# Performance work log

Hardware: AMD Instinct MI355X
Metric: run time of the kernel (lower is better)

The kernel has to match this reference:

```python
import jax, jax.numpy as jnp
import numpy as np

# Dims (match init_kwargs / input_specs)
B, N, DIM, HEADS, DHEAD, CHUNK = 1, 2048, 1024, 8, 128, 64
HID = 4 * DHEAD            # MemoryMLP expansion_factor=4.0
DI = HEADS * DHEAD         # dim_inner
EPS = 1e-6
MAX_LR = 1.0               # default_step_transform_max_lr


def rmsnorm(x, w):
    return x * jax.lax.rsqrt(jnp.mean(jnp.square(x), -1, keepdims=True) + EPS) * w


def mem_forward(w0, w1, g, x):
    # ResidualNorm(MemoryMLP): y = RMSNorm(gelu(x@w0)@w1)*g + x
    h = jax.nn.gelu(x @ w0, approximate=False) @ w1
    return rmsnorm(h, g) + x


def setup_inputs() -> dict:
    key = jax.random.key(0)
    ks = jax.random.split(key, 12)
    s = lambda i, shape, sc: jax.random.normal(ks[i], shape, jnp.float32) * sc
    return dict(
        x=s(0, (B, N, DIM), 1.0),
        store_norm_w=jnp.ones((DIM,), jnp.float32),
        ret_norm_w=jnp.ones((DIM,), jnp.float32),
        Wq=s(1, (DIM, DI), DIM ** -0.5),
        Wk=s(2, (DIM, DI), DIM ** -0.5),
        Wv=s(3, (DIM, DI), DIM ** -0.5),
        W_step=s(4, (DIM, HEADS), DIM ** -0.5), b_step=jnp.zeros((HEADS,), jnp.float32),
        W_mom=s(5, (DIM, HEADS), DIM ** -0.5), b_mom=jnp.zeros((HEADS,), jnp.float32),
        W_decay=s(6, (DIM, HEADS), DIM ** -0.5), b_decay=jnp.zeros((HEADS,), jnp.float32),
        gate_W=s(7, (DIM, HEADS), DIM ** -0.5),
        combine_W=s(8, (DI, DIM), DI ** -0.5),
        mem_w0=s(9, (HEADS, DHEAD, HID), DHEAD ** -0.5),
        mem_w1=s(10, (HEADS, HID, DHEAD), HID ** -0.5),
        mem_g=jnp.ones((HEADS, DHEAD), jnp.float32),
    )


def reference(x, store_norm_w, ret_norm_w, Wq, Wk, Wv, W_step, b_step,
              W_mom, b_mom, W_decay, b_decay, gate_W, combine_W,
              mem_w0, mem_w1, mem_g):
    b, n, _ = x.shape
    nc = n // CHUNK
    BH = b * HEADS

    # ---- store path ----
    s = rmsnorm(x, store_norm_w)                                 # b n dim
    lr = jax.nn.sigmoid(s @ W_step + b_step) * MAX_LR            # b n h (per-token adaptive step)
    pooled = s.reshape(b, nc, CHUNK, DIM).mean(2)                # b nc dim (AveragePool chunk rep)
    mom = jax.nn.sigmoid(pooled @ W_mom + b_mom)                 # b nc h
    dec = jax.nn.sigmoid(pooled @ W_decay + b_decay)             # b nc h

    def to_chunks(t):  # b n (h d) -> (b h) nc c d
        return t.reshape(b, nc, CHUNK, HEADS, DHEAD).transpose(0, 3, 1, 2, 4).reshape(BH, nc, CHUNK, DHEAD)

    k = to_chunks(s @ Wk)
    v = to_chunks(s @ Wv)
    lr_c = lr.reshape(b, nc, CHUNK, HEADS).transpose(0, 3, 1, 2).reshape(BH, nc, CHUNK)
    mom_bh = mom.transpose(0, 2, 1).reshape(BH, nc)
    dec_bh = dec.transpose(0, 2, 1).reshape(BH, nc)

    # init fast weights per (b h)  (per_head_learned_parameters=True)
    w0 = jnp.broadcast_to(mem_w0[None], (b, HEADS, DHEAD, HID)).reshape(BH, DHEAD, HID)
    w1 = jnp.broadcast_to(mem_w1[None], (b, HEADS, HID, DHEAD)).reshape(BH, HID, DHEAD)
    g = jnp.broadcast_to(mem_g[None], (b, HEADS, DHEAD)).reshape(BH, DHEAD)

    def chunk_loss(w0_, w1_, g_, kc, vc, lrc):
        pred = mem_forward(w0_, w1_, g_, kc)                     # c d
        return jnp.sum(jnp.mean(jnp.square(pred - vc), -1) * lrc)

    grad_chunk = jax.grad(chunk_loss, argnums=(0, 1, 2))
    # vmap over chunks (same weights per chunk, per-sample grads), then over (b h)
    grads = jax.vmap(jax.vmap(grad_chunk, in_axes=(None, None, None, 0, 0, 0)))(w0, w1, g, k, v, lr_c)
    surprises = tuple(-gr for gr in grads)                       # each (BH, nc, ...)

    def combine(a, c):
        ga, xa = a
        gb, xb = c
        return (ga * gb, gb * xa + xb)

    def lin_scan(gates, xs):
        # y_i = gates_i * y_{i-1} + xs_i over chunk axis (axis=1)
        return jax.lax.associative_scan(combine, (gates, xs), axis=1)

    def expand(gates, ref):
        return gates.reshape(gates.shape + (1,) * (ref.ndim - 2))

    # momentum scan per parameter tensor
    updates = tuple(lin_scan(expand(mom_bh, su), su)[1] for su in surprises)

    # weight update scan: W_i = (1 - decay_i) * W_{i-1} + momentum_i, W_{-1} = init
    per_chunk_weights = []
    for upd, w_init in zip(updates, (w0, w1, g)):
        gates = expand(1.0 - dec_bh, upd)
        cumg, y = lin_scan(gates, upd)
        w_seq = y + cumg * w_init[:, None]                       # (BH, nc, ...)
        # retrieval at chunk i uses weights updated through chunk i-1
        per_chunk_weights.append(jnp.concatenate([w_init[:, None], w_seq[:, :-1]], axis=1))
    w0_c, w1_c, g_c = per_chunk_weights

    # ---- retrieve path ----
    r = rmsnorm(x, ret_norm_w)
    q = to_chunks(r @ Wq)                                        # (BH, nc, c, d)
    pred = jax.vmap(jax.vmap(mem_forward))(w0_c, w1_c, g_c, q)   # (BH, nc, c, d)
    out = pred.reshape(b, HEADS, n, DHEAD)                       # b h n d
    gate = jax.nn.sigmoid(r @ gate_W)                            # b n h (retrieve_gate, heads>1)
    out = out * gate.transpose(0, 2, 1)[..., None]
    out = out.transpose(0, 2, 1, 3).reshape(b, n, DI) @ combine_W
    return out
```

## Files before the change

### kernel.cpp

```cpp
#include <hip/hip_runtime.h>
#include <hip/hip_bf16.h>
#include <math.h>

#define NH   8
#define DHD  128
#define HIDN 512
#define CHK  64
#define NCH  32
#define MB   1048576ull

typedef unsigned short u16;
typedef unsigned int   u32;
typedef short s16x8 __attribute__((ext_vector_type(8)));
typedef float f32x4 __attribute__((ext_vector_type(4)));

#define MFMA(a,b,c) __builtin_amdgcn_mfma_f32_16x16x32_bf16((a),(b),(c),0,0,0)

__device__ __forceinline__ float bf2f(u16 v){ return __uint_as_float(((u32)v) << 16); }
__device__ __forceinline__ u16 f2bf(float f){
  u32 u = __float_as_uint(f);
  u += 0x7fffu + ((u >> 16) & 1u);
  return (u16)(u >> 16);
}
__device__ __forceinline__ u32 pack2(float a, float b){
  return (u32)f2bf(a) | ((u32)f2bf(b) << 16);
}
__device__ __forceinline__ float waveRedSum(float v){
  #pragma unroll
  for (int off = 32; off; off >>= 1) v += __shfl_xor(v, off);
  return v;
}
__device__ __forceinline__ int swzb(int row, int colb){ return colb ^ ((row & 7) << 4); }
__device__ __forceinline__ int swza(int row, int colb){
  return colb ^ ((row & 7) << 4) ^ (((row >> 3) & 3) << 5);
}



__global__ __launch_bounds__(256) void k_rmsnorm(const float* __restrict__ x,
    const float* __restrict__ wst, const float* __restrict__ wrt,
    u16* __restrict__ s_bf, u16* __restrict__ r_bf){
  int row = blockIdx.x, t = threadIdx.x;
  float4 v = ((const float4*)(x + (size_t)row*1024))[t];
  float ss = v.x*v.x + v.y*v.y + v.z*v.z + v.w*v.w;
  ss = waveRedSum(ss);
  __shared__ float red[4];
  int wv = t >> 6, ln = t & 63;
  if (ln == 0) red[wv] = ss;
  __syncthreads();
  float rr = rsqrtf((red[0]+red[1]+red[2]+red[3])*(1.f/1024.f) + 1e-6f);
  float4 a = ((const float4*)wst)[t];
  float4 b = ((const float4*)wrt)[t];
  uint2 so = make_uint2(pack2(v.x*rr*a.x, v.y*rr*a.y), pack2(v.z*rr*a.z, v.w*rr*a.w));
  uint2 ro = make_uint2(pack2(v.x*rr*b.x, v.y*rr*b.y), pack2(v.z*rr*b.z, v.w*rr*b.w));
  *(uint2*)(s_bf + (size_t)row*1024 + t*4) = so;
  *(uint2*)(r_bf + (size_t)row*1024 + t*4) = ro;
}

__global__ __launch_bounds__(256) void k_pool(const u16* __restrict__ s_bf, float* __restrict__ pooled){
  int c = blockIdx.x; int d = blockIdx.y*256 + threadIdx.x;
  float acc = 0.f;
  for (int tt = 0; tt < 64; ++tt) acc += bf2f(s_bf[((size_t)c*64+tt)*1024 + d]);
  pooled[(size_t)c*1024 + d] = acc * (1.f/64.f);
}

__global__ __launch_bounds__(256) void k_lrgate(const u16* __restrict__ s_bf, const u16* __restrict__ r_bf,
    const float* __restrict__ Wstep, const float* __restrict__ bstep,
    const float* __restrict__ gateW,
    float* __restrict__ lrc, float* __restrict__ gate){
  int wv = threadIdx.x >> 6, ln = threadIdx.x & 63;
  int tok = blockIdx.x*4 + wv;
  const u16* srow = s_bf + (size_t)tok*1024;
  const u16* rrow = r_bf + (size_t)tok*1024;
  for (int o = 0; o < 16; ++o){
    int h = o & 7;
    const u16* src = (o < 8) ? srow : rrow;
    const float* W = (o < 8) ? Wstep : gateW;
    float acc = 0.f;
    for (int k = ln; k < 1024; k += 64) acc += bf2f(src[k])*W[(size_t)k*8+h];
    acc = waveRedSum(acc);
    if (ln == 0){
      if (o < 8){
        float v = 1.f/(1.f+expf(-(acc + bstep[h])));
        lrc[((size_t)h*NCH + (tok>>6))*CHK + (tok&63)] = v;
      } else {
        gate[(size_t)tok*8 + h] = 1.f/(1.f+expf(-acc));
      }
    }
  }
}

__global__ __launch_bounds__(64) void k_momdec(const float* __restrict__ pooled,
    const float* __restrict__ Wmom, const float* __restrict__ bmom,
    const float* __restrict__ Wdec, const float* __restrict__ bdec,
    float* __restrict__ momb, float* __restrict__ decb){
  int c = blockIdx.x, ln = threadIdx.x;
  const float* prow = pooled + (size_t)c*1024;
  for (int o = 0; o < 16; ++o){
    int h = o & 7;
    const float* W = (o < 8) ? Wmom : Wdec;
    float acc = 0.f;
    for (int k = ln; k < 1024; k += 64) acc += prow[k]*W[(size_t)k*8+h];
    acc = waveRedSum(acc);
    if (ln == 0){
      float bb = (o < 8) ? bmom[h] : bdec[h];
      float v = 1.f/(1.f+expf(-(acc+bb)));
      if (o < 8) momb[h*NCH + c] = v; else decb[h*NCH + c] = v;
    }
  }
}

__global__ __launch_bounds__(256) void k_trf4(
    const float* __restrict__ A0, const float* __restrict__ A1,
    const float* __restrict__ A2, const float* __restrict__ A3,
    u16* __restrict__ O0, u16* __restrict__ O1, u16* __restrict__ O2, u16* __restrict__ O3){
  __shared__ u16 tile[32][34];
  int z = blockIdx.z;
  const float* in = (z==0)?A0:(z==1)?A1:(z==2)?A2:A3;
  u16* out = (z==0)?O0:(z==1)?O1:(z==2)?O2:O3;
  int c0 = blockIdx.x*32, r0 = blockIdx.y*32;
  int tx = threadIdx.x & 31, ty = threadIdx.x >> 5;
  #pragma unroll
  for (int k = 0; k < 4; ++k) tile[ty+k*8][tx] = f2bf(in[(size_t)(r0+ty+k*8)*1024 + c0+tx]);
  __syncthreads();
  #pragma unroll
  for (int k = 0; k < 4; ++k) out[(size_t)(c0+ty+k*8)*1024 + r0+tx] = tile[tx][ty+k*8];
}

__global__ __launch_bounds__(256) void k_packw(const float* __restrict__ mw0, const float* __restrict__ mw1,
    u16* __restrict__ w0L, u16* __restrict__ w1L, u16* __restrict__ w1bL){
  int h = blockIdx.z, which = blockIdx.y;
  int i = blockIdx.x*256 + threadIdx.x;
  int r = i & 511, blk = i >> 9;
  int lg = r >> 7, lr = (r >> 3) & 15, e = r & 7;
  float v; u16* dst;
  if (which == 0){ int n0 = blk >> 2, ks = blk & 3; int hid = n0*16+lr, d = ks*32+lg*8+e;
    v = mw0[(size_t)h*65536 + (size_t)d*512 + hid]; dst = w0L; }
  else if (which == 1){ int n0 = blk >> 4, ks = blk & 15; int d = n0*16+lr, hid = ks*32+lg*8+e;
    v = mw1[(size_t)h*65536 + (size_t)hid*128 + d]; dst = w1L; }
  else { int n0 = blk >> 2, ks = blk & 3; int hid = n0*16+lr, d = ks*32+lg*8+e;
    v = mw1[(size_t)h*65536 + (size_t)hid*128 + d]; dst = w1bL; }
  dst[(size_t)h*65536 + i] = f2bf(v);
}

__device__ __forceinline__ void gemm_body(const u16* __restrict__ A, const u16* __restrict__ BT,
    void* __restrict__ Cp, int mode){
  __shared__ char As[8192];
  __shared__ char Bs[8192];
  int t = threadIdx.x; int l = t & 63, w = t >> 6, lr16 = l & 15, lg = l >> 4;
  int bm = blockIdx.x*64, bn = blockIdx.y*64;
  f32x4 acc[4];
  #pragma unroll
  for (int mt = 0; mt < 4; ++mt) acc[mt] = (f32x4){0.f,0.f,0.f,0.f};
  for (int k0 = 0; k0 < 1024; k0 += 64){
    #pragma unroll
    for (int i = 0; i < 2; ++i){ int e = (i*256+t)*8; int row = e>>6, col = e&63;
      *(s16x8*)(As + row*128 + swzb(row, col*2)) = *(const s16x8*)(A + (size_t)(bm+row)*1024 + k0 + col);
      *(s16x8*)(Bs + row*128 + swzb(row, col*2)) = *(const s16x8*)(BT + (size_t)(bn+row)*1024 + k0 + col); }
    __syncthreads();
    #pragma unroll
    for (int ks = 0; ks < 2; ++ks){
      int rowb = w*16 + lr16;
      s16x8 y = *(const s16x8*)(Bs + rowb*128 + swzb(rowb, (ks*32+lg*8)*2));
      #pragma unroll
      for (int mt = 0; mt < 4; ++mt){ int row = mt*16 + lr16;
        s16x8 xa = *(const s16x8*)(As + row*128 + swzb(row, (ks*32+lg*8)*2));
        acc[mt] = MFMA(xa, y, acc[mt]); }
    }
    __syncthreads();
  }
  #pragma unroll
  for (int mt = 0; mt < 4; ++mt)
    #pragma unroll
    for (int j = 0; j < 4; ++j){
      int row = bm + mt*16 + lg*4 + j;
      int coln = bn + w*16 + lr16;
      if (mode == 0) ((float*)Cp)[(size_t)row*1024 + coln] = acc[mt][j];
      else { int cI = row>>6, tok = row&63, h = coln>>7, d = coln&127;
        ((u16*)Cp)[((size_t)(h*32+cI)*64 + tok)*128 + d] = f2bf(acc[mt][j]); }
    }
}

__global__ __launch_bounds__(256) void k_gemm_bf(const u16* __restrict__ A, const u16* __restrict__ BT,
    void* __restrict__ Cp, int mode){ gemm_body(A, BT, Cp, mode); }

__global__ __launch_bounds__(256) void k_gemm3(
    const u16* __restrict__ s_bf, const u16* __restrict__ r_bf,
    const u16* __restrict__ WkT, const u16* __restrict__ WvT, const u16* __restrict__ WqT,
    u16* __restrict__ Kc, u16* __restrict__ Vc, u16* __restrict__ Qc){
  int z = blockIdx.z;
  const u16* A = (z==2) ? r_bf : s_bf;
  const u16* BT = (z==0) ? WkT : (z==1) ? WvT : WqT;
  u16* C = (z==0) ? Kc : (z==1) ? Vc : Qc;
  gemm_body(A, BT, (void*)C, 1);
}

__global__ __launch_bounds__(512) void k_grad(
    const u16* __restrict__ Kc, const u16* __restrict__ Vc, const float* __restrict__ lrc,
    const u16* __restrict__ w0L, const u16* __restrict__ w1L, const u16* __restrict__ w1bL,
    const float* __restrict__ mg,
    u16* __restrict__ SW0, u16* __restrict__ SW1, float* __restrict__ SG){
  extern __shared__ char sm[];
  char* a_s   = sm;
  char* upT_s = sm + 65536;
  char* dh_s  = sm + 131072;
  char* dhT_s = sm + 147456;
  char* duT_s = a_s;
  char* kcT_s = upT_s;
  char* stg3  = dh_s;
  float* scr  = (float*)dh_s;

  int c = blockIdx.x, bh = blockIdx.y, t = threadIdx.x;
  size_t bc = (size_t)bh*NCH + c;
  int l = t & 63, w = t >> 6, lr16 = l & 15, lg = l >> 4;
  int tg = w & 3, dhf = w >> 2;
  int tokb = tg*16, tok0 = tokb + lg*4;

  const u16* kc_g = Kc + bc*8192;
  const u16* vc_g = Vc + bc*8192;

  s16x8 xk[4];
  #pragma unroll
  for (int k = 0; k < 4; ++k)
    xk[k] = *(const s16x8*)(kc_g + (size_t)(tokb+lr16)*128 + k*32 + lg*8);
  const u16* w0Lh = w0L + (size_t)bh*65536;
  for (int n0h = 0; n0h < 16; ++n0h){
    int n0 = dhf*16 + n0h;
    f32x4 acc = {0.f,0.f,0.f,0.f};
    const u16* yb = w0Lh + (size_t)n0*2048 + l*8;
    #pragma unroll
    for (int k = 0; k < 4; ++k) acc = MFMA(xk[k], *(const s16x8*)(yb + k*512), acc);
    int hid = n0*16 + lr16;
    float upv[4];
    #pragma unroll
    for (int j = 0; j < 4; ++j){
      int tok = tok0 + j;
      float u = acc[j];
      float cdf = 0.5f*(1.f + erff(u*0.70710678118654752f));
      upv[j] = cdf + u*0.3989422804014327f*expf(-0.5f*u*u);
      *(u16*)(a_s + tok*1024 + swza(tok, hid*2)) = f2bf(u*cdf);
    }
    *(uint2*)(upT_s + hid*128 + swzb(hid, tok0*2)) =
        make_uint2(pack2(upv[0], upv[1]), pack2(upv[2], upv[3]));
  }
  __syncthreads();

  s16x8 xa[16];
  #pragma unroll
  for (int k = 0; k < 16; ++k){ int row = tokb + lr16;
    xa[k] = *(const s16x8*)(a_s + row*1024 + swza(row, (k*32+lg*8)*2)); }
  const u16* w1Lh = w1L + (size_t)bh*65536;
  f32x4 hD[4];
  #pragma unroll
  for (int n0l = 0; n0l < 4; ++n0l){
    f32x4 acc = {0.f,0.f,0.f,0.f};
    const u16* yb = w1Lh + (size_t)(dhf*4 + n0l)*8192 + l*8;
    #pragma unroll
    for (int k = 0; k < 16; ++k) acc = MFMA(xa[k], *(const s16x8*)(yb + k*512), acc);
    hD[n0l] = acc;
  }
  #pragma unroll
  for (int j = 0; j < 4; ++j){
    float s = 0.f;
    #pragma unroll
    for (int n0l = 0; n0l < 4; ++n0l) s += hD[n0l][j]*hD[n0l][j];
    s += __shfl_xor(s,1); s += __shfl_xor(s,2); s += __shfl_xor(s,4); s += __shfl_xor(s,8);
    if (lr16 == 0) scr[dhf*64 + tok0 + j] = s;
  }
  __syncthreads();
  float rv[4], lrv[4], dotp[4];
  #pragma unroll
  for (int j = 0; j < 4; ++j){
    int tok = tok0 + j;
    float tot = scr[tok] + scr[64 + tok];
    rv[j] = rsqrtf(tot*(1.f/128.f) + 1e-6f);
    lrv[j] = lrc[bc*64 + tok];
    dotp[j] = 0.f;
  }
  float dn[4][4];
  #pragma unroll
  for (int n0l = 0; n0l < 4; ++n0l){
    int d = dhf*64 + n0l*16 + lr16;
    float g0 = mg[(size_t)bh*128 + d];
    float dgav = 0.f;
    #pragma unroll
    for (int j = 0; j < 4; ++j){
      int tok = tok0 + j;
      float h = hD[n0l][j];
      float nrm = h*rv[j];
      float kcv = bf2f(kc_g[(size_t)tok*128 + d]);
      float vcv = bf2f(vc_g[(size_t)tok*128 + d]);
      float p = nrm*g0 + kcv;
      float dp = (2.f/128.f)*lrv[j]*(p - vcv);
      dgav += dp*nrm;
      float dnv = dp*g0;
      dn[n0l][j] = dnv;
      dotp[j] += dnv*h;
    }
    dgav += __shfl_xor(dgav,16); dgav += __shfl_xor(dgav,32);
    if (lg == 0) scr[256 + w*64 + n0l*16 + lr16] = dgav;
  }
  #pragma unroll
  for (int j = 0; j < 4; ++j){
    float dd = dotp[j];
    dd += __shfl_xor(dd,1); dd += __shfl_xor(dd,2); dd += __shfl_xor(dd,4); dd += __shfl_xor(dd,8);
    if (lr16 == 0) scr[128 + dhf*64 + tok0 + j] = dd;
  }
  __syncthreads();
  float dotv[4];
  #pragma unroll
  for (int j = 0; j < 4; ++j){
    int tok = tok0 + j;
    dotv[j] = scr[128 + tok] + scr[128 + 64 + tok];
  }
  if (t < 128){
    int dh2 = t >> 6, dl = t & 63;
    float s = scr[256 + (dh2*4+0)*64 + dl] + scr[256 + (dh2*4+1)*64 + dl]
            + scr[256 + (dh2*4+2)*64 + dl] + scr[256 + (dh2*4+3)*64 + dl];
    SG[bc*128 + t] = -s;
  }
  __syncthreads();
  #pragma unroll
  for (int n0l = 0; n0l < 4; ++n0l){
    int d = dhf*64 + n0l*16 + lr16;
    float dhv[4];
    #pragma unroll
    for (int j = 0; j < 4; ++j){
      int tok = tok0 + j;
      float c3 = rv[j]*rv[j]*rv[j]*(1.f/128.f);
      dhv[j] = rv[j]*dn[n0l][j] - c3*dotv[j]*hD[n0l][j];
      *(u16*)(dh_s + tok*256 + swzb(tok, d*2)) = f2bf(dhv[j]);
    }
    *(uint2*)(dhT_s + d*128 + swzb(d, tok0*2)) =
        make_uint2(pack2(dhv[0], dhv[1]), pack2(dhv[2], dhv[3]));
  }
  __syncthreads();

  {
    s16x8 yB[4][2];
    #pragma unroll
    for (int n0l = 0; n0l < 4; ++n0l){
      int hid = w*64 + n0l*16 + lr16;
      #pragma unroll
      for (int ks = 0; ks < 2; ++ks){
        s16x8 v;
        #pragma unroll
        for (int e = 0; e < 8; ++e){ int tok = ks*32 + lg*8 + e;
          v[e] = *(const short*)(a_s + tok*1024 + swza(tok, hid*2)); }
        yB[n0l][ks] = v;
      }
    }
    __syncthreads();
    u16* stg = (u16*)(a_s + w*8192);
    #pragma unroll 1
    for (int half = 0; half < 2; ++half){
      #pragma unroll
      for (int mt4 = 0; mt4 < 4; ++mt4){
        int mt = half*4 + mt4; int row = mt*16 + lr16;
        s16x8 xD0 = *(const s16x8*)(dhT_s + row*128 + swzb(row, (lg*8)*2));
        s16x8 xD1 = *(const s16x8*)(dhT_s + row*128 + swzb(row, (32+lg*8)*2));
        #pragma unroll
        for (int n0l = 0; n0l < 4; ++n0l){
          f32x4 acc = {0.f,0.f,0.f,0.f};
          acc = MFMA(xD0, yB[n0l][0], acc);
          acc = MFMA(xD1, yB[n0l][1], acc);
          int base = mt4*1024 + (n0l>>1)*512 + (((n0l*2)+(lr16>>3))&3)*128 + (lr16&7);
          #pragma unroll
          for (int j = 0; j < 4; ++j)
            stg[base + (lg*4+j)*8] = f2bf(-acc[j]);
        }
      }
      asm volatile("s_waitcnt lgkmcnt(0)" ::: "memory");
      #pragma unroll
      for (int mt4 = 0; mt4 < 4; ++mt4){
        int mt = half*4 + mt4;
        u16* gb = SW1 + bc*65536 + (size_t)(mt*16 + w*2)*512;
        s16x8 o0 = *(const s16x8*)(stg + mt4*1024 + l*16);
        s16x8 o1 = *(const s16x8*)(stg + mt4*1024 + l*16 + 8);
        *(s16x8*)(gb + l*16) = o0;
        *(s16x8*)(gb + l*16 + 8) = o1;
      }
    }
  }
  __syncthreads();

  {
    s16x8 xDh[4][4];
    #pragma unroll
    for (int mt = 0; mt < 4; ++mt){ int row = mt*16 + lr16;
      #pragma unroll
      for (int ks = 0; ks < 4; ++ks)
        xDh[mt][ks] = *(const s16x8*)(dh_s + row*256 + swzb(row, (ks*32+lg*8)*2)); }
    const u16* w1bh = w1bL + (size_t)bh*65536;
    #pragma unroll 2
    for (int n0l = 0; n0l < 4; ++n0l){
      int hid = w*64 + n0l*16 + lr16;
      s16x8 yW[4];
      const u16* xb = w1bh + (size_t)(w*4 + n0l)*2048 + l*8;
      #pragma unroll
      for (int ks = 0; ks < 4; ++ks)
        yW[ks] = *(const s16x8*)(xb + ks*512);
      #pragma unroll
      for (int mt = 0; mt < 4; ++mt){
        f32x4 acc = {0.f,0.f,0.f,0.f};
        #pragma unroll
        for (int ks = 0; ks < 4; ++ks) acc = MFMA(xDh[mt][ks], yW[ks], acc);
        int tk0 = mt*16 + lg*4;
        uint2 ur = *(const uint2*)(upT_s + hid*128 + swzb(hid, tk0*2));
        float u0 = bf2f((u16)(ur.x & 0xffff)), u1 = bf2f((u16)(ur.x >> 16));
        float u2 = bf2f((u16)(ur.y & 0xffff)), u3 = bf2f((u16)(ur.y >> 16));
        *(uint2*)(duT_s + hid*128 + swzb(hid, tk0*2)) =
            make_uint2(pack2(acc[0]*u0, acc[1]*u1), pack2(acc[2]*u2, acc[3]*u3));
      }
    }
  }
  __syncthreads();

  #pragma unroll
  for (int i = 0; i < 2; ++i){
    int idx = i*512 + t;
    int tok = idx & 63, d0 = (idx >> 6)*8;
    s16x8 kv = *(const s16x8*)(kc_g + (size_t)tok*128 + d0);
    #pragma unroll
    for (int e = 0; e < 8; ++e)
      *(u16*)(kcT_s + (d0+e)*128 + swzb(d0+e, tok*2)) = kv[e];
  }
  __syncthreads();

  {
    s16x8 yK[8][2];
    #pragma unroll
    for (int n0 = 0; n0 < 8; ++n0){
      int d = n0*16 + lr16;
      #pragma unroll
      for (int ks = 0; ks < 2; ++ks)
        yK[n0][ks] = *(const s16x8*)(kcT_s + d*128 + swzb(d, (ks*32+lg*8)*2));
    }
    u16* stg = (u16*)(stg3 + w*4096);
    #pragma unroll 1
    for (int mi = 0; mi < 4; ++mi){
      int hid = w*64 + mi*16 + lr16;
      s16x8 xU0 = *(const s16x8*)(duT_s + hid*128 + swzb(hid, (lg*8)*2));
      s16x8 xU1 = *(const s16x8*)(duT_s + hid*128 + swzb(hid, (32+lg*8)*2));
      #pragma unroll
      for (int n0 = 0; n0 < 8; ++n0){
        f32x4 acc = {0.f,0.f,0.f,0.f};
        acc = MFMA(xU0, yK[n0][0], acc);
        acc = MFMA(xU1, yK[n0][1], acc);
        int base = (n0>>1)*512 + (((n0*2)+(lr16>>3))&3)*128 + (lr16&7);
        #pragma unroll
        for (int j = 0; j < 4; ++j)
          stg[base + (lg*4+j)*8] = f2bf(-acc[j]);
      }
      asm volatile("s_waitcnt lgkmcnt(0)" ::: "memory");
      u16* gb = SW0 + bc*65536 + (size_t)(w*4 + mi)*2048;
      #pragma unroll
      for (int q = 0; q < 4; ++q){
        s16x8 o = *(const s16x8*)(stg + l*32 + q*8);
        *(s16x8*)(gb + l*32 + q*8) = o;
      }
    }
  }
}

__global__ __launch_bounds__(256) void k_scan(
    const u16* __restrict__ w0L, const u16* __restrict__ w1L, const float* __restrict__ mg,
    const u16* __restrict__ SW0, const u16* __restrict__ SW1, const float* __restrict__ SG,
    const float* __restrict__ momb, const float* __restrict__ decb,
    u16* __restrict__ W0C, u16* __restrict__ W1C, float* __restrict__ GC){
  int bh = blockIdx.y;
  int e = blockIdx.x*256 + threadIdx.x;
  const float* momp = momb + bh*NCH;
  const float* decp = decb + bh*NCH;
  float m = 0.f, Wv;
  if (e < 65536){
    Wv = bf2f(w0L[(size_t)bh*65536 + e]);
    const u16* su = SW0 + (size_t)bh*NCH*65536 + e;
    u16* outp = W0C + (size_t)bh*NCH*65536 + e;
    for (int c = 0; c < NCH; ++c){
      outp[(size_t)c*65536] = f2bf(Wv);
      m = momp[c]*m + bf2f(su[(size_t)c*65536]);
      Wv = (1.f - decp[c])*Wv + m;
    }
  } else if (e < 131072){
    int e2 = e - 65536;
    Wv = bf2f(w1L[(size_t)bh*65536 + e2]);
    const u16* su = SW1 + (size_t)bh*NCH*65536 + e2;
    u16* outp = W1C + (size_t)bh*NCH*65536 + e2;
    for (int c = 0; c < NCH; ++c){
      outp[(size_t)c*65536] = f2bf(Wv);
      m = momp[c]*m + bf2f(su[(size_t)c*65536]);
      Wv = (1.f - decp[c])*Wv + m;
    }
  } else if (e < 131200){
    int e3 = e - 131072;
    Wv = mg[(size_t)bh*128 + e3];
    const float* su = SG + (size_t)bh*NCH*128 + e3;
    float* outp = GC + (size_t)bh*NCH*128 + e3;
    for (int c = 0; c < NCH; ++c){
      outp[(size_t)c*128] = Wv;
      m = momp[c]*m + su[(size_t)c*128];
      Wv = (1.f - decp[c])*Wv + m;
    }
  }
}

__global__ __launch_bounds__(512) void k_retr(
    const u16* __restrict__ Qc, const u16* __restrict__ W0C, const u16* __restrict__ W1C,
    const float* __restrict__ GC, const float* __restrict__ gate, u16* __restrict__ OH){
  extern __shared__ char sm[];
  char* a_s = sm;
  float* scr = (float*)(sm + 65536);
  int c = blockIdx.x, bh = blockIdx.y, t = threadIdx.x;
  size_t bc = (size_t)bh*NCH + c;
  int l = t & 63, w = t >> 6, lr16 = l & 15, lg = l >> 4;
  int tg = w & 3, dhf = w >> 2;
  const u16* q_g = Qc + bc*8192;

  s16x8 xq[4];
  #pragma unroll
  for (int k = 0; k < 4; ++k)
    xq[k] = *(const s16x8*)(q_g + (size_t)(tg*16+lr16)*128 + k*32 + lg*8);
  const u16* w0c = W0C + bc*65536;
  for (int n0h = 0; n0h < 16; ++n0h){
    int n0 = dhf*16 + n0h;
    f32x4 acc = {0.f,0.f,0.f,0.f};
    const u16* yb = w0c + (size_t)n0*2048 + l*8;
    #pragma unroll
    for (int k = 0; k < 4; ++k) acc = MFMA(xq[k], *(const s16x8*)(yb + k*512), acc);
    int hid = n0*16 + lr16;
    #pragma unroll
    for (int j = 0; j < 4; ++j){
      int tok = tg*16 + lg*4 + j;
      float u = acc[j];
      float av = u*0.5f*(1.f + erff(u*0.70710678118654752f));
      *(u16*)(a_s + tok*1024 + swza(tok, hid*2)) = f2bf(av);
    }
  }
  __syncthreads();
  s16x8 xa[16];
  #pragma unroll
  for (int k = 0; k < 16; ++k){ int row = tg*16 + lr16;
    xa[k] = *(const s16x8*)(a_s + row*1024 + swza(row, (k*32+lg*8)*2)); }
  const u16* w1c = W1C + bc*65536;
  f32x4 hD[4];
  #pragma unroll
  for (int n0l = 0; n0l < 4; ++n0l){
    f32x4 acc = {0.f,0.f,0.f,0.f};
    const u16* yb = w1c + (size_t)(dhf*4 + n0l)*8192 + l*8;
    #pragma unroll
    for (int k = 0; k < 16; ++k) acc = MFMA(xa[k], *(const s16x8*)(yb + k*512), acc);
    hD[n0l] = acc;
  }
  #pragma unroll
  for (int j = 0; j < 4; ++j){
    float s = 0.f;
    #pragma unroll
    for (int n0l = 0; n0l < 4; ++n0l) s += hD[n0l][j]*hD[n0l][j];
    s += __shfl_xor(s,1); s += __shfl_xor(s,2); s += __shfl_xor(s,4); s += __shfl_xor(s,8);
    if (lr16 == 0) scr[dhf*64 + tg*16 + lg*4 + j] = s;
  }
  __syncthreads();
  float rv[4], gtv[4];
  #pragma unroll
  for (int j = 0; j < 4; ++j){
    int tok = tg*16 + lg*4 + j;
    rv[j] = rsqrtf((scr[tok] + scr[64 + tok])*(1.f/128.f) + 1e-6f);
    gtv[j] = gate[(size_t)(c*64 + tok)*8 + bh];
  }
  #pragma unroll
  for (int n0l = 0; n0l < 4; ++n0l){
    int d = dhf*64 + n0l*16 + lr16;
    float g0 = GC[bc*128 + d];
    #pragma unroll
    for (int j = 0; j < 4; ++j){
      int tok = tg*16 + lg*4 + j; int tokg = c*64 + tok;
      float qv = bf2f(q_g[(size_t)tok*128 + d]);
      float p = hD[n0l][j]*rv[j]*g0 + qv;
      OH[(size_t)tokg*1024 + bh*128 + d] = f2bf(p*gtv[j]);
    }
  }
}

extern "C" void kernel_launch(void* const* d_in, const int* in_sizes, int n_in,
                              void* d_out, int out_size, void* d_ws, size_t ws_size,
                              hipStream_t stream) {
  (void)in_sizes; (void)n_in; (void)out_size; (void)ws_size;
  const float* x     = (const float*)d_in[0];
  const float* snw   = (const float*)d_in[1];
  const float* rnw   = (const float*)d_in[2];
  const float* Wq    = (const float*)d_in[3];
  const float* Wk    = (const float*)d_in[4];
  const float* Wv    = (const float*)d_in[5];
  const float* Wstep = (const float*)d_in[6];
  const float* bstep = (const float*)d_in[7];
  const float* Wmom  = (const float*)d_in[8];
  const float* bmom  = (const float*)d_in[9];
  const float* Wdec  = (const float*)d_in[10];
  const float* bdec  = (const float*)d_in[11];
  const float* gateW = (const float*)d_in[12];
  const float* combW = (const float*)d_in[13];
  const float* mw0   = (const float*)d_in[14];
  const float* mw1   = (const float*)d_in[15];
  const float* mg    = (const float*)d_in[16];
  float* out = (float*)d_out;

  char* Wb = (char*)d_ws;
  u16* Qc    = (u16*)(Wb + 0*MB);
  u16* Kc    = (u16*)(Wb + 4*MB);
  u16* Vc    = (u16*)(Wb + 8*MB);
  u16* s_bf  = (u16*)(Wb + 12*MB);
  u16* r_bf  = (u16*)(Wb + 16*MB);
  u16* WqT   = (u16*)(Wb + 20*MB);
  u16* WkT   = (u16*)(Wb + 22*MB);
  u16* WvT   = (u16*)(Wb + 24*MB);
  u16* combT = (u16*)(Wb + 26*MB);
  u16* w0L   = (u16*)(Wb + 28*MB);
  u16* w1L   = (u16*)(Wb + 29*MB);
  u16* w1bL  = (u16*)(Wb + 30*MB);
  u16* OH    = (u16*)(Wb + 31*MB);
  u16* SW0   = (u16*)(Wb + 35*MB);
  u16* SW1   = (u16*)(Wb + 67*MB);
  u16* W0C   = (u16*)(Wb + 99*MB);
  u16* W1C   = (u16*)(Wb + 131*MB);
  float* pooled = (float*)(Wb + 163*MB);
  float* lrc    = (float*)(Wb + 163*MB + 131072);
  float* momb   = (float*)(Wb + 163*MB + 196608);
  float* decb   = (float*)(Wb + 163*MB + 197632);
  float* gate   = (float*)(Wb + 163*MB + 198656);
  float* SG     = (float*)(Wb + 163*MB + 264192);
  float* GC     = (float*)(Wb + 163*MB + 395264);

  hipFuncSetAttribute((const void*)k_grad, hipFuncAttributeMaxDynamicSharedMemorySize, 163840);
  hipFuncSetAttribute((const void*)k_retr, hipFuncAttributeMaxDynamicSharedMemorySize, 66560);

  k_rmsnorm<<<2048, 256, 0, stream>>>(x, snw, rnw, s_bf, r_bf);
  k_pool<<<dim3(32,4), 256, 0, stream>>>(s_bf, pooled);
  k_lrgate<<<512, 256, 0, stream>>>(s_bf, r_bf, Wstep, bstep, gateW, lrc, gate);
  k_momdec<<<32, 64, 0, stream>>>(pooled, Wmom, bmom, Wdec, bdec, momb, decb);
  k_trf4<<<dim3(32,32,4), 256, 0, stream>>>(Wq, Wk, Wv, combW, WqT, WkT, WvT, combT);
  k_packw<<<dim3(256,3,8), 256, 0, stream>>>(mw0, mw1, w0L, w1L, w1bL);
  k_gemm3<<<dim3(32,16,3), 256, 0, stream>>>(s_bf, r_bf, WkT, WvT, WqT, Kc, Vc, Qc);
  k_grad<<<dim3(32,8), 512, 163840, stream>>>(Kc, Vc, lrc, w0L, w1L, w1bL, mg, SW0, SW1, SG);
  k_scan<<<dim3(513,8), 256, 0, stream>>>(w0L, w1L, mg, SW0, SW1, SG, momb, decb, W0C, W1C, GC);
  k_retr<<<dim3(32,8), 512, 66560, stream>>>(Qc, W0C, W1C, GC, gate, OH);
  k_gemm_bf<<<dim3(32,16), 256, 0, stream>>>(OH, combT, (void*)out, 0);
}
```

Baseline: 271.5 us.

## Retile projection GEMMs to 64x128 with direct-to-LDS loads; vectorize lr/gate projection

The shared GEMM body now uses 512-thread blocks computing 64x128 tiles, with a 2x4 wave grid each doing 2x2 MFMA tiles. Tiles are staged with global_load_lds straight into an unswizzled LDS layout instead of going through registers. The lr/gate projection reads a bf16 weight matrix pre-packed by k_packw, so each lane does 16-element vector dot products instead of strided scalar float loads. The change aims to cut register staging and uncoalesced weight reads, at the cost of possible LDS bank conflicts from the lost swizzle and an extra packing pass.

```diff
diff --git a/kernel.cpp b/kernel.cpp
--- a/kernel.cpp
+++ b/kernel.cpp
@@ -25,10 +25,19 @@
 __device__ __forceinline__ u32 pack2(float a, float b){
   return (u32)f2bf(a) | ((u32)f2bf(b) << 16);
 }
+__device__ __forceinline__ float dot2(u32 a, u32 b){
+  return __uint_as_float(a << 16)*__uint_as_float(b << 16)
+       + __uint_as_float(a & 0xffff0000u)*__uint_as_float(b & 0xffff0000u);
+}
 __device__ __forceinline__ float waveRedSum(float v){
   #pragma unroll
   for (int off = 32; off; off >>= 1) v += __shfl_xor(v, off);
   return v;
+}
+__device__ __forceinline__ void gload16(const void* g, void* l){
+  __builtin_amdgcn_global_load_lds(
+      (const __attribute__((address_space(1))) u32*)g,
+      (__attribute__((address_space(3))) u32*)l, 16, 0, 0);
 }
 __device__ __forceinline__ int swzb(int row, int colb){ return colb ^ ((row & 7) << 4); }
 __device__ __forceinline__ int swza(int row, int colb){
@@ -65,21 +74,24 @@
 }
 
 __global__ __launch_bounds__(256) void k_lrgate(const u16* __restrict__ s_bf, const u16* __restrict__ r_bf,
-    const float* __restrict__ Wstep, const float* __restrict__ bstep,
-    const float* __restrict__ gateW,
+    const u16* __restrict__ WsgL, const float* __restrict__ bstep,
     float* __restrict__ lrc, float* __restrict__ gate){
   int wv = threadIdx.x >> 6, ln = threadIdx.x & 63;
   int tok = blockIdx.x*4 + wv;
-  const u16* srow = s_bf + (size_t)tok*1024;
-  const u16* rrow = r_bf + (size_t)tok*1024;
+  const u16* sp = s_bf + (size_t)tok*1024 + ln*16;
+  const u16* rp = r_bf + (size_t)tok*1024 + ln*16;
+  uint4 s0 = *(const uint4*)sp, s1 = *(const uint4*)(sp+8);
+  uint4 r0 = *(const uint4*)rp, r1 = *(const uint4*)(rp+8);
+  #pragma unroll 4
   for (int o = 0; o < 16; ++o){
-    int h = o & 7;
-    const u16* src = (o < 8) ? srow : rrow;
-    const float* W = (o < 8) ? Wstep : gateW;
-    float acc = 0.f;
-    for (int k = ln; k < 1024; k += 64) acc += bf2f(src[k])*W[(size_t)k*8+h];
+    const u16* wp = WsgL + (size_t)o*1024 + ln*16;
+    uint4 w0v = *(const uint4*)wp, w1v = *(const uint4*)(wp+8);
+    uint4 a0 = (o < 8) ? s0 : r0, a1 = (o < 8) ? s1 : r1;
+    float acc = dot2(a0.x,w0v.x)+dot2(a0.y,w0v.y)+dot2(a0.z,w0v.z)+dot2(a0.w,w0v.w)
+              + dot2(a1.x,w1v.x)+dot2(a1.y,w1v.y)+dot2(a1.z,w1v.z)+dot2(a1.w,w1v.w);
     acc = waveRedSum(acc);
     if (ln == 0){
+      int h = o & 7;
       if (o < 8){
         float v = 1.f/(1.f+expf(-(acc + bstep[h])));
         lrc[((size_t)h*NCH + (tok>>6))*CHK + (tok&63)] = v;
@@ -128,9 +140,18 @@
 }
 
 __global__ __launch_bounds__(256) void k_packw(const float* __restrict__ mw0, const float* __restrict__ mw1,
-    u16* __restrict__ w0L, u16* __restrict__ w1L, u16* __restrict__ w1bL){
+    const float* __restrict__ Wstep, const float* __restrict__ gateW,
+    u16* __restrict__ w0L, u16* __restrict__ w1L, u16* __restrict__ w1bL, u16* __restrict__ WsgL){
   int h = blockIdx.z, which = blockIdx.y;
   int i = blockIdx.x*256 + threadIdx.x;
+  if (which == 3){
+    if (h == 0 && i < 16384){
+      int o = i >> 10, k = i & 1023;
+      float v = (o < 8) ? Wstep[(size_t)k*8 + o] : gateW[(size_t)k*8 + (o-8)];
+      WsgL[i] = f2bf(v);
+    }
+    return;
+  }
   int r = i & 511, blk = i >> 9;
   int lg = r >> 7, lr = (r >> 3) & 15, e = r & 7;
   float v; u16* dst;
@@ -146,45 +167,54 @@
 __device__ __forceinline__ void gemm_body(const u16* __restrict__ A, const u16* __restrict__ BT,
     void* __restrict__ Cp, int mode){
   __shared__ char As[8192];
-  __shared__ char Bs[8192];
-  int t = threadIdx.x; int l = t & 63, w = t >> 6, lr16 = l & 15, lg = l >> 4;
-  int bm = blockIdx.x*64, bn = blockIdx.y*64;
-  f32x4 acc[4];
-  #pragma unroll
-  for (int mt = 0; mt < 4; ++mt) acc[mt] = (f32x4){0.f,0.f,0.f,0.f};
+  __shared__ char Bs[16384];
+  int t = threadIdx.x, l = t & 63, w = t >> 6, lr16 = l & 15, lg = l >> 4;
+  int wm = w & 1, wn = w >> 1;
+  int bm = blockIdx.x*64, bn = blockIdx.y*128;
+  f32x4 acc[2][2];
+  #pragma unroll
+  for (int mt = 0; mt < 2; ++mt)
+    #pragma unroll
+    for (int nt = 0; nt < 2; ++nt) acc[mt][nt] = (f32x4){0.f,0.f,0.f,0.f};
   for (int k0 = 0; k0 < 1024; k0 += 64){
-    #pragma unroll
-    for (int i = 0; i < 2; ++i){ int e = (i*256+t)*8; int row = e>>6, col = e&63;
-      *(s16x8*)(As + row*128 + swzb(row, col*2)) = *(const s16x8*)(A + (size_t)(bm+row)*1024 + k0 + col);
-      *(s16x8*)(Bs + row*128 + swzb(row, col*2)) = *(const s16x8*)(BT + (size_t)(bn+row)*1024 + k0 + col); }
+    gload16(A  + (size_t)(bm + (t>>3))*1024      + k0 + (t&7)*8, As + w*1024);
+    gload16(BT + (size_t)(bn + (t>>3))*1024      + k0 + (t&7)*8, Bs + w*1024);
+    gload16(BT + (size_t)(bn + 64 + (t>>3))*1024 + k0 + (t&7)*8, Bs + 8192 + w*1024);
     __syncthreads();
     #pragma unroll
     for (int ks = 0; ks < 2; ++ks){
-      int rowb = w*16 + lr16;
-      s16x8 y = *(const s16x8*)(Bs + rowb*128 + swzb(rowb, (ks*32+lg*8)*2));
-      #pragma unroll
-      for (int mt = 0; mt < 4; ++mt){ int row = mt*16 + lr16;
-        s16x8 xa = *(const s16x8*)(As + row*128 + swzb(row, (ks*32+lg*8)*2));
-        acc[mt] = MFMA(xa, y, acc[mt]); }
+      s16x8 xa[2], yb[2];
+      #pragma unroll
+      for (int mt = 0; mt < 2; ++mt){ int row = wm*32 + mt*16 + lr16;
+        xa[mt] = *(const s16x8*)(As + row*128 + ks*64 + lg*16); }
+      #pragma unroll
+      for (int nt = 0; nt < 2; ++nt){ int row = wn*32 + nt*16 + lr16;
+        yb[nt] = *(const s16x8*)(Bs + row*128 + ks*64 + lg*16); }
+      #pragma unroll
+      for (int mt = 0; mt < 2; ++mt)
+        #pragma unroll
+        for (int nt = 0; nt < 2; ++nt) acc[mt][nt] = MFMA(xa[mt], yb[nt], acc[mt][nt]);
     }
     __syncthreads();
   }
   #pragma unroll
-  for (int mt = 0; mt < 4; ++mt)
-    #pragma unroll
-    for (int j = 0; j < 4; ++j){
-      int row = bm + mt*16 + lg*4 + j;
-      int coln = bn + w*16 + lr16;
-      if (mode == 0) ((float*)Cp)[(size_t)row*1024 + coln] = acc[mt][j];
-      else { int cI = row>>6, tok = row&63, h = coln>>7, d = coln&127;
-        ((u16*)Cp)[((size_t)(h*32+cI)*64 + tok)*128 + d] = f2bf(acc[mt][j]); }
-    }
-}
-
-__global__ __launch_bounds__(256) void k_gemm_bf(const u16* __restrict__ A, const u16* __restrict__ BT,
+  for (int mt = 0; mt < 2; ++mt)
+    #pragma unroll
+    for (int nt = 0; nt < 2; ++nt)
+      #pragma unroll
+      for (int j = 0; j < 4; ++j){
+        int row = bm + wm*32 + mt*16 + lg*4 + j;
+        int coln = bn + wn*32 + nt*16 + lr16;
+        if (mode == 0) ((float*)Cp)[(size_t)row*1024 + coln] = acc[mt][nt][j];
+        else { int cI = row>>6, tok = row&63, h = coln>>7, d = coln&127;
+          ((u16*)Cp)[((size_t)(h*32+cI)*64 + tok)*128 + d] = f2bf(acc[mt][nt][j]); }
+      }
+}
+
+__global__ __launch_bounds__(512) void k_gemm_bf(const u16* __restrict__ A, const u16* __restrict__ BT,
     void* __restrict__ Cp, int mode){ gemm_body(A, BT, Cp, mode); }
 
-__global__ __launch_bounds__(256) void k_gemm3(
+__global__ __launch_bounds__(512) void k_gemm3(
     const u16* __restrict__ s_bf, const u16* __restrict__ r_bf,
     const u16* __restrict__ WkT, const u16* __restrict__ WvT, const u16* __restrict__ WqT,
     u16* __restrict__ Kc, u16* __restrict__ Vc, u16* __restrict__ Qc){
@@ -630,19 +660,20 @@
   float* gate   = (float*)(Wb + 163*MB + 198656);
   float* SG     = (float*)(Wb + 163*MB + 264192);
   float* GC     = (float*)(Wb + 163*MB + 395264);
+  u16* WsgL  = (u16*)(Wb + 163*MB + 526336);
 
   hipFuncSetAttribute((const void*)k_grad, hipFuncAttributeMaxDynamicSharedMemorySize, 163840);
   hipFuncSetAttribute((const void*)k_retr, hipFuncAttributeMaxDynamicSharedMemorySize, 66560);
 
   k_rmsnorm<<<2048, 256, 0, stream>>>(x, snw, rnw, s_bf, r_bf);
   k_pool<<<dim3(32,4), 256, 0, stream>>>(s_bf, pooled);
-  k_lrgate<<<512, 256, 0, stream>>>(s_bf, r_bf, Wstep, bstep, gateW, lrc, gate);
+  k_packw<<<dim3(256,4,8), 256, 0, stream>>>(mw0, mw1, Wstep, gateW, w0L, w1L, w1bL, WsgL);
+  k_lrgate<<<512, 256, 0, stream>>>(s_bf, r_bf, WsgL, bstep, lrc, gate);
   k_momdec<<<32, 64, 0, stream>>>(pooled, Wmom, bmom, Wdec, bdec, momb, decb);
   k_trf4<<<dim3(32,32,4), 256, 0, stream>>>(Wq, Wk, Wv, combW, WqT, WkT, WvT, combT);
-  k_packw<<<dim3(256,3,8), 256, 0, stream>>>(mw0, mw1, w0L, w1L, w1bL);
-  k_gemm3<<<dim3(32,16,3), 256, 0, stream>>>(s_bf, r_bf, WkT, WvT, WqT, Kc, Vc, Qc);
+  k_gemm3<<<dim3(32,8,3), 512, 0, stream>>>(s_bf, r_bf, WkT, WvT, WqT, Kc, Vc, Qc);
   k_grad<<<dim3(32,8), 512, 163840, stream>>>(Kc, Vc, lrc, w0L, w1L, w1bL, mg, SW0, SW1, SG);
   k_scan<<<dim3(513,8), 256, 0, stream>>>(w0L, w1L, mg, SW0, SW1, SG, momb, decb, W0C, W1C, GC);
   k_retr<<<dim3(32,8), 512, 66560, stream>>>(Qc, W0C, W1C, GC, gate, OH);
-  k_gemm_bf<<<dim3(32,16), 256, 0, stream>>>(OH, combT, (void*)out, 0);
-}
+  k_gemm_bf<<<dim3(32,8), 512, 0, stream>>>(OH, combT, (void*)out, 0);
+}
```

Measured after the change: 228.3 us. 15.9% less time.
